# Kernel tuning notes

Measured on AMD Instinct MI355X. Metric: run time of the kernel, lower is better.

## Reference

```python
import jax, jax.numpy as jnp
import numpy as np

B, L, D, U = 8, 512, 128, 32
ATT_WIDTH = 128
EPS = 1e-7  # K.epsilon()


def setup_inputs() -> dict:
    key = jax.random.key(0)
    ks = jax.random.split(key, 4)
    x = jax.random.normal(ks[0], (B, L, D), dtype=jnp.float32)
    Wt = jax.random.normal(ks[1], (D, U), dtype=jnp.float32) * 0.1
    Wx = jax.random.normal(ks[2], (D, U), dtype=jnp.float32) * 0.1
    bh = jnp.zeros((U,), dtype=jnp.float32)
    Wa = jax.random.normal(ks[3], (U, 1), dtype=jnp.float32) * 0.1
    ba = jnp.zeros((1,), dtype=jnp.float32)
    return {"x": x, "Wt": Wt, "Wx": Wx, "bh": bh, "Wa": Wa, "ba": ba}


def reference(x, Wt, Wx, bh, Wa, ba):
    # Additive attention scores: e[b,t,s] = Wa^T (x_t Wt + x_s Wx + bh) + ba
    q = x @ Wt                              # [B,L,U]
    k = x @ Wx                              # [B,L,U]
    h = q[:, :, None, :] + k[:, None, :, :] + bh   # [B,L,L,U]
    e = jnp.einsum('btsu,u->bts', h, Wa[:, 0]) + ba[0]  # [B,L,L]
    # Windowed mask (non-causal): key j visible to query i iff lower[j] <= i < upper[j]
    lower = jnp.arange(L) - ATT_WIDTH // 2
    upper = lower + ATT_WIDTH
    idx = jnp.arange(L)[:, None]
    mask = (idx >= lower) & (idx < upper)   # [L,L]
    # Original zeroes masked scores (NOT -inf) before softmax — keep that.
    e = jnp.where(mask[None, :, :], e, jnp.zeros_like(e))
    e = e - jnp.max(e, axis=-1, keepdims=True)
    a = jnp.exp(e)
    a = a / (jnp.sum(a, axis=-1, keepdims=True) + EPS)  # [B,L,L]
    v = jnp.einsum('bts,bsd->btd', a, x)    # [B,L,D]
    return v
```

## Files before the change

kernel.cpp:

```cpp
#include <hip/hip_runtime.h>
#include <float.h>

#define B 8
#define L 512
#define D 128
#define U 32
#define WIN 128
#define EPS 1e-7f
#define T 4
#define ROWS (T + WIN - 1)
#define WP 9

__global__ __launch_bounds__(256) void prep_kernel(
        const float* __restrict__ x, const float* __restrict__ Wt,
        const float* __restrict__ Wx, const float* __restrict__ bh,
        const float* __restrict__ Wa, const float* __restrict__ ba,
        float* __restrict__ xpart, float* __restrict__ wqk) {
    __shared__ float red[256];
    int blk = blockIdx.x, tid = threadIdx.x;
    int b = blk >> 3, j = blk & 7;
    int d = tid & 127, h = tid >> 7;
    const float* xp = x + ((size_t)(b * L + j * 64 + h * 32)) * D + d;
    float s = 0.f;
#pragma unroll 8
    for (int i = 0; i < 32; ++i) s += xp[(size_t)i * D];
    red[tid] = s;
    __syncthreads();
    if (tid < 128) xpart[blk * 128 + tid] = red[tid] + red[tid + 128];

    if (blk == 0) {
        if (tid < 128) {
            float sq = 0.f;
#pragma unroll
            for (int u = 0; u < U; ++u) sq += Wt[tid * U + u] * Wa[u];
            wqk[tid] = sq;
        } else {
            int dd = tid - 128;
            float sk = 0.f;
#pragma unroll
            for (int u = 0; u < U; ++u) sk += Wx[dd * U + u] * Wa[u];
            wqk[128 + dd] = sk;
        }
        if (tid == 0) {
            float s2 = ba[0];
            for (int u = 0; u < U; ++u) s2 += bh[u] * Wa[u];
            wqk[256] = s2;
        }
    }
}

__global__ __launch_bounds__(256) void attn_kernel(
        const float* __restrict__ x, const float* __restrict__ wqk,
        const float* __restrict__ xpart, float* __restrict__ out) {
    __shared__ float swq[D], swk[D];
    __shared__ float kds[ROWS];
    __shared__ float qds[T];
    __shared__ float w[ROWS * WP];
    __shared__ float adj[T];
    int blk = blockIdx.x;
    int b = blk >> 7;
    int t0 = (blk & 127) * T;
    int row0 = t0 - (WIN / 2 - 1);
    int tid = threadIdx.x;
    int rlo = max(0, -row0);
    int rhi = min(ROWS, L - row0);

    if (tid < 128) swq[tid] = wqk[tid];
    else           swk[tid - 128] = wqk[tid];
    float cval = wqk[256];
    for (int i = tid; i < ROWS * WP; i += 256) w[i] = 0.f;
    __syncthreads();

    const float4* xb4 = (const float4*)(x + (size_t)b * L * D);

#pragma unroll
    for (int pass = 0; pass < 2; ++pass) {
        int r = pass * 128 + (tid >> 1);
        int h = tid & 1;
        if (r < ROWS && r >= rlo && r < rhi) {
            const float4* xr = xb4 + (size_t)(row0 + r) * (D / 4) + h * 16;
            float sq = 0.f, sk = 0.f;
            int d0 = h * 64;
#pragma unroll
            for (int i = 0; i < 16; ++i) {
                float4 v = xr[i];
                sq += v.x * swq[d0+4*i]   + v.y * swq[d0+4*i+1]
                    + v.z * swq[d0+4*i+2] + v.w * swq[d0+4*i+3];
                sk += v.x * swk[d0+4*i]   + v.y * swk[d0+4*i+1]
                    + v.z * swk[d0+4*i+2] + v.w * swk[d0+4*i+3];
            }
            sq += __shfl_xor(sq, 1);
            sk += __shfl_xor(sk, 1);
            if (h == 0) {
                kds[r] = sk;
                int qi = r - (WIN / 2 - 1);
                if (qi >= 0 && qi < T) qds[qi] = sq + cval;
            }
        }
    }
    __syncthreads();

    {
        int q = tid >> 6, kt = tid & 63;
        int t = t0 + q;
        float qv = qds[q];
        float e[2];
        int   sv[2];
#pragma unroll
        for (int i = 0; i < 2; ++i) {
            int r = q + kt + 64 * i;
            bool valid = (r >= rlo) && (r < rhi);
            sv[i] = valid;
            e[i] = valid ? (qv + kds[r]) : -FLT_MAX;
        }
        float mx = fmaxf(e[0], e[1]);
#pragma unroll
        for (int off = 32; off > 0; off >>= 1) mx = fmaxf(mx, __shfl_xor(mx, off));
        float m = fmaxf(mx, 0.f);
        float w0 = __expf(-m);
        float wv[2], sm = 0.f;
#pragma unroll
        for (int i = 0; i < 2; ++i) {
            wv[i] = sv[i] ? __expf(e[i] - m) : 0.f;
            sm += wv[i];
        }
#pragma unroll
        for (int off = 32; off > 0; off >>= 1) sm += __shfl_xor(sm, off);
        int ss0 = max(0, t - 63), ss1 = min(L, t + 65);
        int count = ss1 - ss0;
        float inv = 1.f / (sm + (float)(L - count) * w0 + EPS);
#pragma unroll
        for (int i = 0; i < 2; ++i) {
            int r = q + kt + 64 * i;
            if (sv[i]) w[r * WP + q] = (wv[i] - w0) * inv;
        }
        if (kt == 0) adj[q] = w0 * inv;
    }
    __syncthreads();

    {
        int q = tid >> 6, h = (tid >> 5) & 1, dt = tid & 31;
        int mid = rlo + ((rhi - rlo + 1) >> 1);
        int ra = h ? mid : rlo;
        int rb = h ? rhi : mid;
        float4 acc = {0.f, 0.f, 0.f, 0.f};
#pragma unroll 4
        for (int r = ra; r < rb; ++r) {
            float4 xv = xb4[(size_t)(row0 + r) * (D / 4) + dt];
            float ww = w[r * WP + q];
            acc.x += ww * xv.x; acc.y += ww * xv.y;
            acc.z += ww * xv.z; acc.w += ww * xv.w;
        }
        acc.x += __shfl_xor(acc.x, 32); acc.y += __shfl_xor(acc.y, 32);
        acc.z += __shfl_xor(acc.z, 32); acc.w += __shfl_xor(acc.w, 32);

        if (h == 0) {
            const float4* xp = (const float4*)(xpart + (size_t)(8 * b) * D);
            float sx = 0.f, sy = 0.f, sz = 0.f, sw = 0.f;
#pragma unroll
            for (int j = 0; j < 8; ++j) {
                float4 v = xp[j * 32 + dt];
                sx += v.x; sy += v.y; sz += v.z; sw += v.w;
            }
            float a = adj[q];
            float4 o = {acc.x + a * sx, acc.y + a * sy,
                        acc.z + a * sz, acc.w + a * sw};
            ((float4*)out)[((size_t)(b * L + t0 + q)) * (D / 4) + dt] = o;
        }
    }
}

extern "C" void kernel_launch(void* const* d_in, const int* in_sizes, int n_in,
                              void* d_out, int out_size, void* d_ws, size_t ws_size,
                              hipStream_t stream) {
    const float* x  = (const float*)d_in[0];
    const float* Wt = (const float*)d_in[1];
    const float* Wx = (const float*)d_in[2];
    const float* bh = (const float*)d_in[3];
    const float* Wa = (const float*)d_in[4];
    const float* ba = (const float*)d_in[5];
    float* out = (float*)d_out;

    float* ws    = (float*)d_ws;
    float* xpart = ws;
    float* wqk   = xpart + 64 * 128;

    prep_kernel<<<64, 256, 0, stream>>>(x, Wt, Wx, bh, Wa, ba, xpart, wqk);
    attn_kernel<<<B * (L / T), 256, 0, stream>>>(x, wqk, xpart, out);
}
```

Before: 87.96 us.

## Precompute per-row q/k scores once in prep kernel instead of per attention block

Moves the per-row dot products of x with the folded query and key vectors out of the attention kernel into the prep kernel, which now computes them once per row and writes them to workspace. Before, each attention block recomputed these for its 131-row window, so every row was reduced about 32 times. The attention kernel now reads the scalars from global memory, and its shared-memory weight padding is reduced. In exchange, the prep kernel does more work per block and every block now redundantly recomputes the folded weight vectors.

```diff
diff --git a/kernel.cpp b/kernel.cpp
--- a/kernel.cpp
+++ b/kernel.cpp
@@ -9,52 +9,84 @@
 #define EPS 1e-7f
 #define T 4
 #define ROWS (T + WIN - 1)
-#define WP 9
+#define WP 5
 
 __global__ __launch_bounds__(256) void prep_kernel(
         const float* __restrict__ x, const float* __restrict__ Wt,
         const float* __restrict__ Wx, const float* __restrict__ bh,
         const float* __restrict__ Wa, const float* __restrict__ ba,
-        float* __restrict__ xpart, float* __restrict__ wqk) {
-    __shared__ float red[256];
+        float* __restrict__ qd, float* __restrict__ kd,
+        float* __restrict__ xpart) {
+    __shared__ float swq[D], swk[D];
+    __shared__ float4 red4[8][32];
     int blk = blockIdx.x, tid = threadIdx.x;
-    int b = blk >> 3, j = blk & 7;
-    int d = tid & 127, h = tid >> 7;
-    const float* xp = x + ((size_t)(b * L + j * 64 + h * 32)) * D + d;
-    float s = 0.f;
-#pragma unroll 8
-    for (int i = 0; i < 32; ++i) s += xp[(size_t)i * D];
-    red[tid] = s;
+    int row0 = blk * 64;
+
+    if (tid < 128) {
+        float sq = 0.f;
+#pragma unroll
+        for (int u = 0; u < U; ++u) sq += Wt[tid * U + u] * Wa[u];
+        swq[tid] = sq;
+    } else {
+        int dd = tid - 128;
+        float sk = 0.f;
+#pragma unroll
+        for (int u = 0; u < U; ++u) sk += Wx[dd * U + u] * Wa[u];
+        swk[dd] = sk;
+    }
+    float cval = ba[0];
+#pragma unroll
+    for (int u = 0; u < U; ++u) cval += bh[u] * Wa[u];
     __syncthreads();
-    if (tid < 128) xpart[blk * 128 + tid] = red[tid] + red[tid + 128];
 
-    if (blk == 0) {
-        if (tid < 128) {
-            float sq = 0.f;
+    {
+        int rl = tid >> 2, qr = tid & 3;
+        int row = row0 + rl;
+        const float4* xr = (const float4*)(x + (size_t)row * D) + qr * 8;
+        float sq = 0.f, sk = 0.f;
+        int d0 = qr * 32;
 #pragma unroll
-            for (int u = 0; u < U; ++u) sq += Wt[tid * U + u] * Wa[u];
-            wqk[tid] = sq;
-        } else {
-            int dd = tid - 128;
-            float sk = 0.f;
+        for (int i = 0; i < 8; ++i) {
+            float4 v = xr[i];
+            sq += v.x * swq[d0+4*i]   + v.y * swq[d0+4*i+1]
+                + v.z * swq[d0+4*i+2] + v.w * swq[d0+4*i+3];
+            sk += v.x * swk[d0+4*i]   + v.y * swk[d0+4*i+1]
+                + v.z * swk[d0+4*i+2] + v.w * swk[d0+4*i+3];
+        }
+        sq += __shfl_xor(sq, 1); sq += __shfl_xor(sq, 2);
+        sk += __shfl_xor(sk, 1); sk += __shfl_xor(sk, 2);
+        if (qr == 0) { qd[row] = sq + cval; kd[row] = sk; }
+    }
+
+    {
+        int c4 = tid & 31, rg = tid >> 5;
+        const float4* xp = (const float4*)(x + (size_t)(row0 + rg * 8) * D) + c4;
+        float4 s = {0.f, 0.f, 0.f, 0.f};
 #pragma unroll
-            for (int u = 0; u < U; ++u) sk += Wx[dd * U + u] * Wa[u];
-            wqk[128 + dd] = sk;
+        for (int i = 0; i < 8; ++i) {
+            float4 v = xp[(size_t)i * (D / 4)];
+            s.x += v.x; s.y += v.y; s.z += v.z; s.w += v.w;
         }
-        if (tid == 0) {
-            float s2 = ba[0];
-            for (int u = 0; u < U; ++u) s2 += bh[u] * Wa[u];
-            wqk[256] = s2;
+        red4[rg][c4] = s;
+    }
+    __syncthreads();
+#pragma unroll
+    for (int off = 4; off > 0; off >>= 1) {
+        int c4 = tid & 31, rg = tid >> 5;
+        if (rg < off) {
+            float4 a = red4[rg][c4], bb = red4[rg + off][c4];
+            a.x += bb.x; a.y += bb.y; a.z += bb.z; a.w += bb.w;
+            red4[rg][c4] = a;
         }
+        __syncthreads();
     }
+    if (tid < 32) ((float4*)(xpart + (size_t)blk * D))[tid] = red4[0][tid];
 }
 
 __global__ __launch_bounds__(256) void attn_kernel(
-        const float* __restrict__ x, const float* __restrict__ wqk,
-        const float* __restrict__ xpart, float* __restrict__ out) {
-    __shared__ float swq[D], swk[D];
-    __shared__ float kds[ROWS];
-    __shared__ float qds[T];
+        const float* __restrict__ x, const float* __restrict__ qd,
+        const float* __restrict__ kd, const float* __restrict__ xpart,
+        float* __restrict__ out) {
     __shared__ float w[ROWS * WP];
     __shared__ float adj[T];
     int blk = blockIdx.x;
@@ -65,45 +97,13 @@
     int rlo = max(0, -row0);
     int rhi = min(ROWS, L - row0);
 
-    if (tid < 128) swq[tid] = wqk[tid];
-    else           swk[tid - 128] = wqk[tid];
-    float cval = wqk[256];
     for (int i = tid; i < ROWS * WP; i += 256) w[i] = 0.f;
-    __syncthreads();
-
-    const float4* xb4 = (const float4*)(x + (size_t)b * L * D);
-
-#pragma unroll
-    for (int pass = 0; pass < 2; ++pass) {
-        int r = pass * 128 + (tid >> 1);
-        int h = tid & 1;
-        if (r < ROWS && r >= rlo && r < rhi) {
-            const float4* xr = xb4 + (size_t)(row0 + r) * (D / 4) + h * 16;
-            float sq = 0.f, sk = 0.f;
-            int d0 = h * 64;
-#pragma unroll
-            for (int i = 0; i < 16; ++i) {
-                float4 v = xr[i];
-                sq += v.x * swq[d0+4*i]   + v.y * swq[d0+4*i+1]
-                    + v.z * swq[d0+4*i+2] + v.w * swq[d0+4*i+3];
-                sk += v.x * swk[d0+4*i]   + v.y * swk[d0+4*i+1]
-                    + v.z * swk[d0+4*i+2] + v.w * swk[d0+4*i+3];
-            }
-            sq += __shfl_xor(sq, 1);
-            sk += __shfl_xor(sk, 1);
-            if (h == 0) {
-                kds[r] = sk;
-                int qi = r - (WIN / 2 - 1);
-                if (qi >= 0 && qi < T) qds[qi] = sq + cval;
-            }
-        }
-    }
     __syncthreads();
 
     {
         int q = tid >> 6, kt = tid & 63;
         int t = t0 + q;
-        float qv = qds[q];
+        float qv = qd[b * L + t];
         float e[2];
         int   sv[2];
 #pragma unroll
@@ -111,7 +111,7 @@
             int r = q + kt + 64 * i;
             bool valid = (r >= rlo) && (r < rhi);
             sv[i] = valid;
-            e[i] = valid ? (qv + kds[r]) : -FLT_MAX;
+            e[i] = valid ? (qv + kd[b * L + row0 + r]) : -FLT_MAX;
         }
         float mx = fmaxf(e[0], e[1]);
 #pragma unroll
@@ -143,6 +143,7 @@
         int mid = rlo + ((rhi - rlo + 1) >> 1);
         int ra = h ? mid : rlo;
         int rb = h ? rhi : mid;
+        const float4* xb4 = (const float4*)(x + (size_t)b * L * D);
         float4 acc = {0.f, 0.f, 0.f, 0.f};
 #pragma unroll 4
         for (int r = ra; r < rb; ++r) {
@@ -182,9 +183,10 @@
     float* out = (float*)d_out;
 
     float* ws    = (float*)d_ws;
-    float* xpart = ws;
-    float* wqk   = xpart + 64 * 128;
+    float* qd    = ws;
+    float* kd    = qd + B * L;
+    float* xpart = kd + B * L;
 
-    prep_kernel<<<64, 256, 0, stream>>>(x, Wt, Wx, bh, Wa, ba, xpart, wqk);
-    attn_kernel<<<B * (L / T), 256, 0, stream>>>(x, wqk, xpart, out);
+    prep_kernel<<<64, 256, 0, stream>>>(x, Wt, Wx, bh, Wa, ba, qd, kd, xpart);
+    attn_kernel<<<B * (L / T), 256, 0, stream>>>(x, qd, kd, xpart, out);
 }
```

New measurement: 80.03 us. 9.0% less time.
